# Optimization experiments

Measured on AMD Instinct MI355X. Metric: run time of the kernel, lower is better.

## Reference

```python
import jax, jax.numpy as jnp
import numpy as np
import math

N_EMBD = 1024
N_HEAD = 16
D_FF = 4 * N_EMBD
B, T = 4, 2048

def gelu_tanh(x):
    return 0.5 * x * (1.0 + jnp.tanh(jnp.sqrt(2.0 / jnp.pi).astype(x.dtype) * (x + 0.044715 * x ** 3)))

def layernorm(x, g, b, eps=1e-5):
    mu = jnp.mean(x, axis=-1, keepdims=True)
    var = jnp.var(x, axis=-1, keepdims=True)
    return (x - mu) * jax.lax.rsqrt(var + eps) * g + b

def setup_inputs() -> dict:
    key = jax.random.key(0)
    ks = jax.random.split(key, 12)
    s = lambda fan_in: 1.0 / np.sqrt(fan_in)
    return {
        "x": jax.random.normal(ks[0], (B, T, N_EMBD), jnp.float32),
        "ln1_g": jnp.ones((N_EMBD,), jnp.float32),
        "ln1_b": jnp.zeros((N_EMBD,), jnp.float32),
        "w_attn": jax.random.normal(ks[1], (N_EMBD, 3 * N_EMBD), jnp.float32) * s(N_EMBD),
        "b_attn": jnp.zeros((3 * N_EMBD,), jnp.float32),
        "w_proj": jax.random.normal(ks[2], (N_EMBD, N_EMBD), jnp.float32) * s(N_EMBD),
        "b_proj": jnp.zeros((N_EMBD,), jnp.float32),
        "ln2_g": jnp.ones((N_EMBD,), jnp.float32),
        "ln2_b": jnp.zeros((N_EMBD,), jnp.float32),
        "w_fc": jax.random.normal(ks[3], (N_EMBD, D_FF), jnp.float32) * s(N_EMBD),
        "b_fc": jnp.zeros((D_FF,), jnp.float32),
        "w_fc2": jax.random.normal(ks[4], (D_FF, N_EMBD), jnp.float32) * s(D_FF),
        "b_fc2": jnp.zeros((N_EMBD,), jnp.float32),
    }

def reference(x, ln1_g, ln1_b, w_attn, b_attn, w_proj, b_proj,
              ln2_g, ln2_b, w_fc, b_fc, w_fc2, b_fc2):
    Bn, Tn, C = x.shape
    hs = C // N_HEAD
    # --- attention ---
    h = layernorm(x, ln1_g, ln1_b)
    qkv = h @ w_attn + b_attn  # [B,T,3C]
    q, k, v = jnp.split(qkv, 3, axis=-1)
    q = q.reshape(Bn, Tn, N_HEAD, hs).transpose(0, 2, 1, 3)
    k = k.reshape(Bn, Tn, N_HEAD, hs).transpose(0, 2, 1, 3)
    v = v.reshape(Bn, Tn, N_HEAD, hs).transpose(0, 2, 1, 3)
    att = jnp.einsum('bhqd,bhkd->bhqk', q, k) * (hs ** -0.5)
    mask = jnp.tril(jnp.ones((Tn, Tn), bool))
    att = jnp.where(mask, att, -jnp.inf)
    att = jax.nn.softmax(att, axis=-1)
    y = jnp.einsum('bhqk,bhkd->bhqd', att, v)
    y = y.transpose(0, 2, 1, 3).reshape(Bn, Tn, C)
    x = x + (y @ w_proj + b_proj)
    # --- MLP ---
    h2 = layernorm(x, ln2_g, ln2_b)
    h2 = gelu_tanh(h2 @ w_fc + b_fc)
    x = x + (h2 @ w_fc2 + b_fc2)
    return x
```

## Files before the change

### kernel.cpp

```cpp
#include <hip/hip_runtime.h>
#include <hip/hip_bf16.h>

#define B_ 4
#define T_ 2048
#define C_ 1024
#define NH_ 16
#define FF_ 4096
#define NT_ (B_*T_)

typedef short bf16x8 __attribute__((ext_vector_type(8)));
typedef float f32x4 __attribute__((ext_vector_type(4)));

#define LDS_AS(p) ((__attribute__((address_space(3))) uint32_t*)(p))
#define GLB_AS(p) ((const __attribute__((address_space(1))) uint32_t*)(p))

__device__ __forceinline__ float bf2f(__hip_bfloat16 v){ return __bfloat162float(v); }
__device__ __forceinline__ __hip_bfloat16 f2bf(float f){ return __float2bfloat16(f); }

__device__ __forceinline__ f32x4 mfma16(bf16x8 a, bf16x8 b, f32x4 c){
  return __builtin_amdgcn_mfma_f32_16x16x32_bf16(a, b, c, 0, 0, 0);
}

__global__ __launch_bounds__(256) void transpose_bf16(const float* __restrict__ in,
                                                      __hip_bfloat16* __restrict__ out,
                                                      int K, int N) {
  __shared__ float tile[32][33];
  const int n0 = blockIdx.x * 32, k0 = blockIdx.y * 32;
  const int x = threadIdx.x & 31, y = threadIdx.x >> 5;
  #pragma unroll
  for (int i = 0; i < 4; i++)
    tile[y + 8*i][x] = in[(size_t)(k0 + y + 8*i) * N + n0 + x];
  __syncthreads();
  #pragma unroll
  for (int i = 0; i < 4; i++)
    out[(size_t)(n0 + y + 8*i) * K + k0 + x] = f2bf(tile[x][y + 8*i]);
}

__global__ __launch_bounds__(256) void ln_bf16(const float* __restrict__ x,
                                               const float* __restrict__ g,
                                               const float* __restrict__ b,
                                               __hip_bfloat16* __restrict__ out) {
  const int row = blockIdx.x;
  const int tid = threadIdx.x;
  float4 v = ((const float4*)(x + (size_t)row * C_))[tid];
  float s  = v.x + v.y + v.z + v.w;
  float s2 = v.x*v.x + v.y*v.y + v.z*v.z + v.w*v.w;
  #pragma unroll
  for (int off = 32; off > 0; off >>= 1) {
    s  += __shfl_down(s,  off, 64);
    s2 += __shfl_down(s2, off, 64);
  }
  __shared__ float red[8];
  const int w = tid >> 6, l = tid & 63;
  if (l == 0) { red[w] = s; red[4 + w] = s2; }
  __syncthreads();
  s  = red[0] + red[1] + red[2] + red[3];
  s2 = red[4] + red[5] + red[6] + red[7];
  const float mu   = s * (1.0f / C_);
  const float var  = s2 * (1.0f / C_) - mu * mu;
  const float rstd = rsqrtf(var + 1e-5f);
  float4 gv = ((const float4*)g)[tid];
  float4 bv = ((const float4*)b)[tid];
  ushort4 o;
  __hip_bfloat16 t;
  t = f2bf((v.x - mu) * rstd * gv.x + bv.x); o.x = *(unsigned short*)&t;
  t = f2bf((v.y - mu) * rstd * gv.y + bv.y); o.y = *(unsigned short*)&t;
  t = f2bf((v.z - mu) * rstd * gv.z + bv.z); o.z = *(unsigned short*)&t;
  t = f2bf((v.w - mu) * rstd * gv.w + bv.w); o.w = *(unsigned short*)&t;
  ((ushort4*)out)[(size_t)row * (C_/4) + tid] = o;
}

template <int MODE>
__global__ __launch_bounds__(256) void gemm_bt(const __hip_bfloat16* __restrict__ A,
                                               const __hip_bfloat16* __restrict__ BT,
                                               const float* __restrict__ bias,
                                               const float* __restrict__ resid,
                                               void* __restrict__ outp,
                                               void* __restrict__ outp2,
                                               int N, int K) {
  __shared__ __hip_bfloat16 Als[128 * 64];
  __shared__ __hip_bfloat16 Bls[128 * 64];
  const int tid = threadIdx.x;
  const int w = tid >> 6, l = tid & 63;
  const int tile_n = blockIdx.x * 128;
  const int tile_m = blockIdx.y * 128;
  const int wm = (w >> 1) * 64, wn = (w & 1) * 64;

  f32x4 acc[4][4] = {};

  const int lrow8 = l >> 3;
  const int gchunk = (l & 7) ^ lrow8;
  const int m_ = (l & 15);
  const int q_ = (l >> 4);

  for (int k0 = 0; k0 < K; k0 += 64) {
    #pragma unroll
    for (int jj = 0; jj < 2; jj++) {
      const int r0 = w*16 + 8*jj + lrow8;
      __builtin_amdgcn_global_load_lds(GLB_AS(A  + (size_t)(tile_m + r0) * K + k0 + gchunk*8),
                                       LDS_AS(&Als[(w*16 + 8*jj) * 64]), 16, 0, 0);
      __builtin_amdgcn_global_load_lds(GLB_AS(A  + (size_t)(tile_m + 64 + r0) * K + k0 + gchunk*8),
                                       LDS_AS(&Als[(64 + w*16 + 8*jj) * 64]), 16, 0, 0);
      __builtin_amdgcn_global_load_lds(GLB_AS(BT + (size_t)(tile_n + r0) * K + k0 + gchunk*8),
                                       LDS_AS(&Bls[(w*16 + 8*jj) * 64]), 16, 0, 0);
      __builtin_amdgcn_global_load_lds(GLB_AS(BT + (size_t)(tile_n + 64 + r0) * K + k0 + gchunk*8),
                                       LDS_AS(&Bls[(64 + w*16 + 8*jj) * 64]), 16, 0, 0);
    }
    __syncthreads();
    bf16x8 af[2][4], bfr[2][4];
    #pragma unroll
    for (int c = 0; c < 2; c++) {
      #pragma unroll
      for (int mi = 0; mi < 4; mi++) {
        const int row = wm + mi*16 + m_;
        af[c][mi] = *(const bf16x8*)&Als[row * 64 + (((c*4 + q_) ^ (row & 7)) * 8)];
      }
      #pragma unroll
      for (int ni = 0; ni < 4; ni++) {
        const int row = wn + ni*16 + m_;
        bfr[c][ni] = *(const bf16x8*)&Bls[row * 64 + (((c*4 + q_) ^ (row & 7)) * 8)];
      }
    }
    #pragma unroll
    for (int c = 0; c < 2; c++)
      #pragma unroll
      for (int mi = 0; mi < 4; mi++)
        #pragma unroll
        for (int ni = 0; ni < 4; ni++)
          acc[mi][ni] = mfma16(af[c][mi], bfr[c][ni], acc[mi][ni]);
    __syncthreads();
  }

  const int r0 = tile_m + wm + q_ * 4;
  const int c0 = tile_n + wn + m_;
  #pragma unroll
  for (int mi = 0; mi < 4; mi++) {
    #pragma unroll
    for (int r = 0; r < 4; r++) {
      const int row = r0 + mi * 16 + r;
      #pragma unroll
      for (int ni = 0; ni < 4; ni++) {
        const int col = c0 + ni * 16;
        float v = acc[mi][ni][r] + bias[col];
        if (MODE == 0) {
          if (tile_n < 2 * C_) {
            ((__hip_bfloat16*)outp)[(size_t)row * (2*C_) + col] = f2bf(v);
          } else {
            const int dg = col - 2 * C_;
            ((__hip_bfloat16*)outp2)[((size_t)((row >> 11) * 1024 + dg)) * T_ + (row & 2047)] = f2bf(v);
          }
        } else if (MODE == 1 || MODE == 3) {
          ((float*)outp)[(size_t)row * N + col] = resid[(size_t)row * N + col] + v;
        } else {
          const float u = 0.7978845608028654f * (v + 0.044715f * v * v * v);
          const float e = __expf(2.0f * u);
          ((__hip_bfloat16*)outp)[(size_t)row * N + col] = f2bf(v * (1.0f - 1.0f / (e + 1.0f)));
        }
      }
    }
  }
}

__global__ __launch_bounds__(256, 4) void flash_attn(const __hip_bfloat16* __restrict__ qk,
                                                     const __hip_bfloat16* __restrict__ vT,
                                                     __hip_bfloat16* __restrict__ y) {
  const int id  = blockIdx.x;
  const int xcd = id & 7;
  const int jj  = id >> 3;
  const int bh  = xcd * 8 + (jj >> 4);
  const int p   = jj & 15;
  const int b   = bh >> 4, h = bh & 15;
  const int tid = threadIdx.x, w = tid >> 6, l = tid & 63;
  const int m_ = l & 15, q_ = l >> 4;
  const int lrow8 = l >> 3;
  const int gchunk = (l & 7) ^ lrow8;

  __shared__ __hip_bfloat16 Kls[2][64 * 64];
  __shared__ __hip_bfloat16 Vls[64 * 64];
  __shared__ __hip_bfloat16 Pls[64 * 76];

  const size_t kgbase = (size_t)b * T_ * (2*C_) + C_ + h*64;
  const size_t vgbase = (size_t)bh * 64 * T_;

#define STAGE_K(kt_, buf_) do {                                                        \
    _Pragma("unroll")                                                                  \
    for (int j2 = 0; j2 < 2; j2++) {                                                   \
      const int rg = j2*32 + w*8;                                                      \
      __builtin_amdgcn_global_load_lds(                                                \
        GLB_AS(qk + kgbase + (size_t)((kt_)*64 + rg + lrow8)*(2*C_) + gchunk*8),       \
        LDS_AS(&Kls[buf_][rg*64]), 16, 0, 0);                                          \
    }                                                                                  \
  } while (0)

#define STAGE_V(kt_) do {                                                              \
    _Pragma("unroll")                                                                  \
    for (int j2 = 0; j2 < 2; j2++) {                                                   \
      const int rg = j2*32 + w*8;                                                      \
      __builtin_amdgcn_global_load_lds(                                                \
        GLB_AS(vT + vgbase + (size_t)(rg + lrow8)*T_ + (kt_)*64 + gchunk*8),           \
        LDS_AS(&Vls[rg*64]), 16, 0, 0);                                                \
    }                                                                                  \
  } while (0)

  #pragma unroll 1
  for (int ui = 0; ui < 2; ui++) {
    const int qt = ui ? (31 - p) : p;
    const int q0 = qt * 64;

    bf16x8 aq[2];
    {
      const float qscale = 0.125f * 1.44269504088896f;
      const size_t qbase = ((size_t)b * T_ + q0 + w*16 + m_) * (2*C_) + h*64;
      #pragma unroll
      for (int kh = 0; kh < 2; kh++) {
        union { uint4 u; __hip_bfloat16 h8[8]; } t;
        t.u = *(const uint4*)&qk[qbase + kh*32 + q_*8];
        __hip_bfloat16 a[8];
        #pragma unroll
        for (int jx = 0; jx < 8; jx++) a[jx] = f2bf(bf2f(t.h8[jx]) * qscale);
        aq[kh] = *(const bf16x8*)a;
      }
    }

    f32x4 accO[4] = {};
    float lsum[4] = {0.f, 0.f, 0.f, 0.f};

    STAGE_K(0, 0);
    asm volatile("s_waitcnt vmcnt(0)" ::: "memory");
    __builtin_amdgcn_s_barrier();

    int cur = 0;
    #pragma unroll 1
    for (int kt = 0; kt <= qt; kt++) {
      STAGE_V(kt);

      f32x4 s[4];
      #pragma unroll
      for (int ni = 0; ni < 4; ni++) {
        const int row = ni*16 + m_;
        const bf16x8 bk0 = *(const bf16x8*)&Kls[cur][row*64 + ((q_     ^ (row & 7)) * 8)];
        const bf16x8 bk1 = *(const bf16x8*)&Kls[cur][row*64 + (((4+q_) ^ (row & 7)) * 8)];
        f32x4 z = {};
        z = mfma16(aq[0], bk0, z);
        s[ni] = mfma16(aq[1], bk1, z);
      }

      if (kt < qt) STAGE_K(kt + 1, cur ^ 1);

      if (kt == qt) {
        const int qrow = w*16 + q_*4;
        #pragma unroll
        for (int ni = 0; ni < 4; ni++) {
          const int kcol = ni*16 + m_;
          #pragma unroll
          for (int r = 0; r < 4; r++)
            if (kcol > qrow + r) s[ni][r] = -1e30f;
        }
      }

      #pragma unroll
      for (int ni = 0; ni < 4; ni++)
        #pragma unroll
        for (int r = 0; r < 4; r++)
          s[ni][r] = exp2f(s[ni][r]);
      #pragma unroll
      for (int r = 0; r < 4; r++)
        lsum[r] += (s[0][r] + s[1][r]) + (s[2][r] + s[3][r]);
      #pragma unroll
      for (int ni = 0; ni < 4; ni++)
        #pragma unroll
        for (int r = 0; r < 4; r++)
          Pls[(w*16 + q_*4 + r) * 76 + ni*16 + m_] = f2bf(s[ni][r]);

      bf16x8 ap[2];
      ap[0] = *(const bf16x8*)&Pls[(w*16 + m_) * 76 + q_*8];
      ap[1] = *(const bf16x8*)&Pls[(w*16 + m_) * 76 + 32 + q_*8];

      if (kt < qt) asm volatile("s_waitcnt vmcnt(2)" ::: "memory");
      else         asm volatile("s_waitcnt vmcnt(0)" ::: "memory");
      __builtin_amdgcn_s_barrier();

      #pragma unroll
      for (int ni = 0; ni < 4; ni++) {
        const int row = ni*16 + m_;
        const bf16x8 bv0 = *(const bf16x8*)&Vls[row*64 + ((q_     ^ (row & 7)) * 8)];
        const bf16x8 bv1 = *(const bf16x8*)&Vls[row*64 + (((4+q_) ^ (row & 7)) * 8)];
        accO[ni] = mfma16(ap[0], bv0, accO[ni]);
        accO[ni] = mfma16(ap[1], bv1, accO[ni]);
      }

      asm volatile("s_waitcnt vmcnt(0) lgkmcnt(0)" ::: "memory");
      __builtin_amdgcn_s_barrier();
      cur ^= 1;
    }

    #pragma unroll
    for (int r = 0; r < 4; r++) {
      #pragma unroll
      for (int d = 1; d < 16; d <<= 1)
        lsum[r] += __shfl_xor(lsum[r], d, 64);
    }

    const size_t ybase = ((size_t)b * T_ + q0) * C_ + h*64;
    #pragma unroll
    for (int r = 0; r < 4; r++) {
      const int row = w*16 + q_*4 + r;
      const float linv = 1.0f / lsum[r];
      #pragma unroll
      for (int ni = 0; ni < 4; ni++)
        y[ybase + (size_t)row * C_ + ni*16 + m_] = f2bf(accO[ni][r] * linv);
    }
  }
#undef STAGE_K
#undef STAGE_V
}

extern "C" void kernel_launch(void* const* d_in, const int* in_sizes, int n_in,
                              void* d_out, int out_size, void* d_ws, size_t ws_size,
                              hipStream_t stream) {
  const float* x      = (const float*)d_in[0];
  const float* ln1_g  = (const float*)d_in[1];
  const float* ln1_b  = (const float*)d_in[2];
  const float* w_attn = (const float*)d_in[3];
  const float* b_attn = (const float*)d_in[4];
  const float* w_proj = (const float*)d_in[5];
  const float* b_proj = (const float*)d_in[6];
  const float* ln2_g  = (const float*)d_in[7];
  const float* ln2_b  = (const float*)d_in[8];
  const float* w_fc   = (const float*)d_in[9];
  const float* b_fc   = (const float*)d_in[10];
  const float* w_fc2  = (const float*)d_in[11];
  const float* b_fc2  = (const float*)d_in[12];
  float* out = (float*)d_out;

  char* ws = (char*)d_ws;
  const size_t MB = 1024 * 1024;
  __hip_bfloat16* h      = (__hip_bfloat16*)(ws);
  __hip_bfloat16* qk     = (__hip_bfloat16*)(ws + 16*MB);
  __hip_bfloat16* vT     = (__hip_bfloat16*)(ws + 48*MB);
  __hip_bfloat16* y      = (__hip_bfloat16*)(ws + 64*MB);
  float*          x2     = (float*)        (ws + 80*MB);
  __hip_bfloat16* h2     = (__hip_bfloat16*)(ws + 64*MB);
  __hip_bfloat16* gbuf   = (__hip_bfloat16*)(ws);
  __hip_bfloat16* wattnT = (__hip_bfloat16*)(ws + 112*MB);
  __hip_bfloat16* wprojT = (__hip_bfloat16*)(ws + 118*MB);
  __hip_bfloat16* wfcT   = (__hip_bfloat16*)(ws + 120*MB);
  __hip_bfloat16* wfc2T  = (__hip_bfloat16*)(ws + 128*MB);

  transpose_bf16<<<dim3(3*C_/32, C_/32), 256, 0, stream>>>(w_attn, wattnT, C_, 3*C_);
  transpose_bf16<<<dim3(C_/32,  C_/32), 256, 0, stream>>>(w_proj, wprojT, C_, C_);
  transpose_bf16<<<dim3(FF_/32, C_/32), 256, 0, stream>>>(w_fc,   wfcT,   C_, FF_);
  transpose_bf16<<<dim3(C_/32, FF_/32), 256, 0, stream>>>(w_fc2,  wfc2T,  FF_, C_);

  ln_bf16<<<NT_, 256, 0, stream>>>(x, ln1_g, ln1_b, h);
  gemm_bt<0><<<dim3(3*C_/128, NT_/128), 256, 0, stream>>>(h, wattnT, b_attn, nullptr, qk, vT, 3*C_, C_);
  flash_attn<<<dim3(1024), 256, 0, stream>>>(qk, vT, y);
  gemm_bt<1><<<dim3(C_/128, NT_/128), 256, 0, stream>>>(y, wprojT, b_proj, x, x2, nullptr, C_, C_);
  ln_bf16<<<NT_, 256, 0, stream>>>(x2, ln2_g, ln2_b, h2);
  gemm_bt<2><<<dim3(FF_/128, NT_/128), 256, 0, stream>>>(h2, wfcT, b_fc, nullptr, gbuf, nullptr, FF_, C_);
  gemm_bt<3><<<dim3(C_/128, NT_/128), 256, 0, stream>>>(gbuf, wfc2T, b_fc2, x2, out, nullptr, C_, FF_);
}
```

Baseline: 538.0 us.

## Use larger double-buffered GEMM tiles with 512 threads and swizzled block order

Replaces the 128x128 single-buffered GEMM with a 512-thread kernel using 128x256 or 256x256 tiles. LDS stages are double-buffered, so the next K-slice loads while the current one is computed, and only one barrier is needed per iteration. Block indices are remapped so neighbouring workgroups share tiles in cache. Larger tiles raise arithmetic intensity and cut global traffic, but they use much more LDS and registers, which may limit occupancy. The proj and fc2 GEMMs now launch only 256 blocks, which could underfill the GPU.

```diff
diff --git a/kernel.cpp b/kernel.cpp
--- a/kernel.cpp
+++ b/kernel.cpp
@@ -70,71 +70,90 @@
   ((ushort4*)out)[(size_t)row * (C_/4) + tid] = o;
 }
 
-template <int MODE>
-__global__ __launch_bounds__(256) void gemm_bt(const __hip_bfloat16* __restrict__ A,
-                                               const __hip_bfloat16* __restrict__ BT,
-                                               const float* __restrict__ bias,
-                                               const float* __restrict__ resid,
-                                               void* __restrict__ outp,
-                                               void* __restrict__ outp2,
-                                               int N, int K) {
-  __shared__ __hip_bfloat16 Als[128 * 64];
-  __shared__ __hip_bfloat16 Bls[128 * 64];
+template <int MODE, int BM>
+__global__ __launch_bounds__(512, 2) void gemm256(const __hip_bfloat16* __restrict__ A,
+                                                  const __hip_bfloat16* __restrict__ BT,
+                                                  const float* __restrict__ bias,
+                                                  const float* __restrict__ resid,
+                                                  void* __restrict__ outp,
+                                                  void* __restrict__ outp2,
+                                                  int N, int K) {
+  constexpr int MF = BM / 32;
+  constexpr int AJ = (BM == 256) ? 4 : 2;
+  __shared__ __hip_bfloat16 Als[2][BM * 64];
+  __shared__ __hip_bfloat16 Bls[2][256 * 64];
   const int tid = threadIdx.x;
   const int w = tid >> 6, l = tid & 63;
-  const int tile_n = blockIdx.x * 128;
-  const int tile_m = blockIdx.y * 128;
-  const int wm = (w >> 1) * 64, wn = (w & 1) * 64;
-
-  f32x4 acc[4][4] = {};
-
+  const int wm = w >> 2, wn = w & 3;
+  const int m_ = l & 15, q_ = l >> 4;
   const int lrow8 = l >> 3;
   const int gchunk = (l & 7) ^ lrow8;
-  const int m_ = (l & 15);
-  const int q_ = (l >> 4);
-
-  for (int k0 = 0; k0 < K; k0 += 64) {
-    #pragma unroll
-    for (int jj = 0; jj < 2; jj++) {
-      const int r0 = w*16 + 8*jj + lrow8;
-      __builtin_amdgcn_global_load_lds(GLB_AS(A  + (size_t)(tile_m + r0) * K + k0 + gchunk*8),
-                                       LDS_AS(&Als[(w*16 + 8*jj) * 64]), 16, 0, 0);
-      __builtin_amdgcn_global_load_lds(GLB_AS(A  + (size_t)(tile_m + 64 + r0) * K + k0 + gchunk*8),
-                                       LDS_AS(&Als[(64 + w*16 + 8*jj) * 64]), 16, 0, 0);
-      __builtin_amdgcn_global_load_lds(GLB_AS(BT + (size_t)(tile_n + r0) * K + k0 + gchunk*8),
-                                       LDS_AS(&Bls[(w*16 + 8*jj) * 64]), 16, 0, 0);
-      __builtin_amdgcn_global_load_lds(GLB_AS(BT + (size_t)(tile_n + 64 + r0) * K + k0 + gchunk*8),
-                                       LDS_AS(&Bls[(64 + w*16 + 8*jj) * 64]), 16, 0, 0);
+
+  const int nwg = gridDim.x;
+  const int bid = blockIdx.x;
+  const int swz = (bid & 7) * (nwg >> 3) + (bid >> 3);
+  const int nbx = N >> 8;
+  const int tile_n = (swz % nbx) * 256;
+  const int tile_m = (swz / nbx) * BM;
+
+  const int arow0 = (BM == 256) ? (wm * 128 + wn * 32) : (wm * 64 + wn * 16);
+  const int brow0 = (wn >> 1) * 128 + (wm * 2 + (wn & 1)) * 32;
+
+  f32x4 acc[MF][4] = {};
+
+#define STAGE256(buf_, k0_) do {                                                   \
+    _Pragma("unroll")                                                              \
+    for (int j = 0; j < AJ; j++) {                                                 \
+      const int rg = arow0 + j*8;                                                  \
+      __builtin_amdgcn_global_load_lds(                                            \
+        GLB_AS(A + (size_t)(tile_m + rg + lrow8) * K + (k0_) + gchunk*8),          \
+        LDS_AS(&Als[buf_][rg*64]), 16, 0, 0);                                      \
+    }                                                                              \
+    _Pragma("unroll")                                                              \
+    for (int j = 0; j < 4; j++) {                                                  \
+      const int rg = brow0 + j*8;                                                  \
+      __builtin_amdgcn_global_load_lds(                                            \
+        GLB_AS(BT + (size_t)(tile_n + rg + lrow8) * K + (k0_) + gchunk*8),         \
+        LDS_AS(&Bls[buf_][rg*64]), 16, 0, 0);                                      \
+    }                                                                              \
+  } while (0)
+
+  STAGE256(0, 0);
+  __syncthreads();
+
+  const int nt = K >> 6;
+  int cur = 0;
+  #pragma unroll 1
+  for (int t = 0; t < nt; t++) {
+    if (t + 1 < nt) STAGE256(cur ^ 1, (t + 1) * 64);
+
+    bf16x8 bfr[2][4];
+    #pragma unroll
+    for (int kc = 0; kc < 2; kc++)
+      #pragma unroll
+      for (int ni = 0; ni < 4; ni++) {
+        const int row = wn*64 + ni*16 + m_;
+        bfr[kc][ni] = *(const bf16x8*)&Bls[cur][row*64 + (((kc*4 + q_) ^ (row & 7)) * 8)];
+      }
+    #pragma unroll
+    for (int mi = 0; mi < MF; mi++) {
+      const int row = wm*(BM/2) + mi*16 + m_;
+      const bf16x8 a0 = *(const bf16x8*)&Als[cur][row*64 + ((q_       ^ (row & 7)) * 8)];
+      const bf16x8 a1 = *(const bf16x8*)&Als[cur][row*64 + (((4 + q_) ^ (row & 7)) * 8)];
+      #pragma unroll
+      for (int ni = 0; ni < 4; ni++) acc[mi][ni] = mfma16(a0, bfr[0][ni], acc[mi][ni]);
+      #pragma unroll
+      for (int ni = 0; ni < 4; ni++) acc[mi][ni] = mfma16(a1, bfr[1][ni], acc[mi][ni]);
     }
     __syncthreads();
-    bf16x8 af[2][4], bfr[2][4];
-    #pragma unroll
-    for (int c = 0; c < 2; c++) {
-      #pragma unroll
-      for (int mi = 0; mi < 4; mi++) {
-        const int row = wm + mi*16 + m_;
-        af[c][mi] = *(const bf16x8*)&Als[row * 64 + (((c*4 + q_) ^ (row & 7)) * 8)];
-      }
-      #pragma unroll
-      for (int ni = 0; ni < 4; ni++) {
-        const int row = wn + ni*16 + m_;
-        bfr[c][ni] = *(const bf16x8*)&Bls[row * 64 + (((c*4 + q_) ^ (row & 7)) * 8)];
-      }
-    }
-    #pragma unroll
-    for (int c = 0; c < 2; c++)
-      #pragma unroll
-      for (int mi = 0; mi < 4; mi++)
-        #pragma unroll
-        for (int ni = 0; ni < 4; ni++)
-          acc[mi][ni] = mfma16(af[c][mi], bfr[c][ni], acc[mi][ni]);
-    __syncthreads();
+    cur ^= 1;
   }
-
-  const int r0 = tile_m + wm + q_ * 4;
-  const int c0 = tile_n + wn + m_;
+#undef STAGE256
+
+  const int r0 = tile_m + wm * (BM/2) + q_ * 4;
+  const int c0 = tile_n + wn * 64 + m_;
   #pragma unroll
-  for (int mi = 0; mi < 4; mi++) {
+  for (int mi = 0; mi < MF; mi++) {
     #pragma unroll
     for (int r = 0; r < 4; r++) {
       const int row = r0 + mi * 16 + r;
@@ -353,10 +372,10 @@
   transpose_bf16<<<dim3(C_/32, FF_/32), 256, 0, stream>>>(w_fc2,  wfc2T,  FF_, C_);
 
   ln_bf16<<<NT_, 256, 0, stream>>>(x, ln1_g, ln1_b, h);
-  gemm_bt<0><<<dim3(3*C_/128, NT_/128), 256, 0, stream>>>(h, wattnT, b_attn, nullptr, qk, vT, 3*C_, C_);
+  gemm256<0,128><<<dim3(768), 512, 0, stream>>>(h, wattnT, b_attn, nullptr, qk, vT, 3*C_, C_);
   flash_attn<<<dim3(1024), 256, 0, stream>>>(qk, vT, y);
-  gemm_bt<1><<<dim3(C_/128, NT_/128), 256, 0, stream>>>(y, wprojT, b_proj, x, x2, nullptr, C_, C_);
+  gemm256<1,128><<<dim3(256), 512, 0, stream>>>(y, wprojT, b_proj, x, x2, nullptr, C_, C_);
   ln_bf16<<<NT_, 256, 0, stream>>>(x2, ln2_g, ln2_b, h2);
-  gemm_bt<2><<<dim3(FF_/128, NT_/128), 256, 0, stream>>>(h2, wfcT, b_fc, nullptr, gbuf, nullptr, FF_, C_);
-  gemm_bt<3><<<dim3(C_/128, NT_/128), 256, 0, stream>>>(gbuf, wfc2T, b_fc2, x2, out, nullptr, C_, FF_);
-}
+  gemm256<2,256><<<dim3(512), 512, 0, stream>>>(h2, wfcT, b_fc, nullptr, gbuf, nullptr, FF_, C_);
+  gemm256<3,128><<<dim3(256), 512, 0, stream>>>(gbuf, wfc2T, b_fc2, x2, out, nullptr, C_, FF_);
+}
```

After: 526.2 us. -2.2%, faster.
